# Kernel optimization log

Measured on AMD Instinct MI355X. Metric: run time of the kernel, lower is better.

The kernel has to match this reference:

```python
import jax, jax.numpy as jnp
import numpy as np
from jax import lax

# Grid / module constants (from init_kwargs)
D = 128        # spatial extent per axis (shape=[128,128,128])
CIN = 16       # in_channels
COUT = 32      # out_channels
K = 2          # kernel_size
S = 2          # stride
B = 2          # batch_size
N = 200000     # number of active voxels


def setup_inputs() -> dict:
    key = jax.random.key(0)
    k1, k2, k3, k4 = jax.random.split(key, 4)
    features = jax.random.normal(k1, (N, CIN), dtype=jnp.float32)
    coors = jax.random.randint(k2, (N, 4), 0, D)                  # [b, z, y, x]
    coors = coors.at[:, 0].set(coors[:, 0] % B)                    # batch ids in [0, B)
    # Learned params: SCN Convolution / Deconvolution weights (bias=False).
    W1 = jax.random.normal(k3, (COUT, CIN, K, K, K), dtype=jnp.float32) * 0.1
    W2 = jax.random.normal(k4, (CIN, COUT, K, K, K), dtype=jnp.float32) * 0.1
    return {"features": features, "W1": W1, "W2": W2, "coors": coors, "batch_size": B}


def reference(features, W1, W2, coors, batch_size):
    # scn.InputLayer: scatter point features onto the sparse voxel grid
    # (duplicate coords are summed). Inactive sites are exactly zero, so a
    # dense strided conv computes the same values as the rulebook
    # gather-GEMM-scatter at every active output site.
    b, z, y, x = coors[:, 0], coors[:, 1], coors[:, 2], coors[:, 3]
    dense = jnp.zeros((batch_size, CIN, D, D, D), dtype=features.dtype)
    dense = dense.at[b, :, z, y, x].add(features)                  # [B, CIN, D, D, D]

    dn = ("NCDHW", "OIDHW", "NCDHW")
    # scn.Convolution(ndim, CIN, COUT, K, S): valid strided conv -> [B, COUT, D//S, ...]
    h = lax.conv_general_dilated(dense, W1, window_strides=(S, S, S),
                                 padding="VALID", dimension_numbers=dn)
    # scn.Deconvolution(ndim, COUT, CIN, K, S): transposed conv back to [B, CIN, D, D, D]
    dec = lax.conv_general_dilated(h, W2, window_strides=(1, 1, 1),
                                   padding=[(K - 1, K - 1)] * 3,
                                   lhs_dilation=(S, S, S), dimension_numbers=dn)
    # Coupled deconv in SCN restores exactly the input active set; SparseToDense
    # then writes zeros everywhere else -> mask to the original active sites.
    mask = jnp.zeros((batch_size, 1, D, D, D), dtype=features.dtype)
    mask = mask.at[b, :, z, y, x].set(1.0)
    return dec * mask
```

## Files before the change

### kernel.cpp

```cpp
#include <hip/hip_runtime.h>


#define NPT_CH_SCATTER 32
#define NPT_CH_GATHER  16

__global__ __launch_bounds__(256) void scn_scatter_conv1(
    const float* __restrict__ feat, const float* __restrict__ W1,
    const int* __restrict__ coors, float* __restrict__ h, int npts)
{
    __shared__ float Ws[8 * 16 * 32];
    for (int i = threadIdx.x; i < 4096; i += 256) {
        int ic = i >> 7, rem = i & 127, cin = rem >> 3, p = rem & 7;
        Ws[(p << 9) | (cin << 5) | ic] = W1[i];
    }
    __syncthreads();

    int total = npts * NPT_CH_SCATTER;
    for (int idx = blockIdx.x * 256 + threadIdx.x; idx < total;
         idx += gridDim.x * 256) {
        int pid = idx >> 5, ic = idx & 31;
        int b = coors[pid * 4 + 0];
        int z = coors[pid * 4 + 1];
        int y = coors[pid * 4 + 2];
        int x = coors[pid * 4 + 3];
        int p = ((z & 1) << 2) | ((y & 1) << 1) | (x & 1);

        const float4* f4 = reinterpret_cast<const float4*>(feat + pid * 16);
        float4 a0 = f4[0], a1 = f4[1], a2 = f4[2], a3 = f4[3];

        const float* w = Ws + (p << 9) + ic;
        float s = 0.f;
        s += a0.x * w[0 << 5];  s += a0.y * w[1 << 5];
        s += a0.z * w[2 << 5];  s += a0.w * w[3 << 5];
        s += a1.x * w[4 << 5];  s += a1.y * w[5 << 5];
        s += a1.z * w[6 << 5];  s += a1.w * w[7 << 5];
        s += a2.x * w[8 << 5];  s += a2.y * w[9 << 5];
        s += a2.z * w[10 << 5]; s += a2.w * w[11 << 5];
        s += a3.x * w[12 << 5]; s += a3.y * w[13 << 5];
        s += a3.z * w[14 << 5]; s += a3.w * w[15 << 5];

        int cell = (b << 18) | ((z >> 1) << 12) | ((y >> 1) << 6) | (x >> 1);
        atomicAdd(&h[((size_t)cell << 5) | ic], s);
    }
}

__global__ __launch_bounds__(256) void scn_gather_deconv2(
    const float* __restrict__ h, const float* __restrict__ W2,
    const int* __restrict__ coors, float* __restrict__ out, int npts)
{
    __shared__ float Ws[8 * 32 * 16];
    for (int i = threadIdx.x; i < 4096; i += 256) {
        int oc = i >> 8, rem = i & 255, ic = rem >> 3, p = rem & 7;
        Ws[(p << 9) | (ic << 4) | oc] = W2[i];
    }
    __syncthreads();

    int total = npts * NPT_CH_GATHER;
    for (int idx = blockIdx.x * 256 + threadIdx.x; idx < total;
         idx += gridDim.x * 256) {
        int pid = idx >> 4, oc = idx & 15;
        int b = coors[pid * 4 + 0];
        int z = coors[pid * 4 + 1];
        int y = coors[pid * 4 + 2];
        int x = coors[pid * 4 + 3];
        int p = (((z & 1) ^ 1) << 2) | (((y & 1) ^ 1) << 1) | ((x & 1) ^ 1);

        int cell = (b << 18) | ((z >> 1) << 12) | ((y >> 1) << 6) | (x >> 1);
        const float4* h4 = reinterpret_cast<const float4*>(h + ((size_t)cell << 5));
        float4 h0 = h4[0], h1 = h4[1], h2 = h4[2], h3 = h4[3];
        float4 h5 = h4[4], h6 = h4[5], h7 = h4[6], h8 = h4[7];

        const float* w = Ws + (p << 9) + oc;
        float s = 0.f;
        s += h0.x * w[0 << 4];   s += h0.y * w[1 << 4];
        s += h0.z * w[2 << 4];   s += h0.w * w[3 << 4];
        s += h1.x * w[4 << 4];   s += h1.y * w[5 << 4];
        s += h1.z * w[6 << 4];   s += h1.w * w[7 << 4];
        s += h2.x * w[8 << 4];   s += h2.y * w[9 << 4];
        s += h2.z * w[10 << 4];  s += h2.w * w[11 << 4];
        s += h3.x * w[12 << 4];  s += h3.y * w[13 << 4];
        s += h3.z * w[14 << 4];  s += h3.w * w[15 << 4];
        s += h5.x * w[16 << 4];  s += h5.y * w[17 << 4];
        s += h5.z * w[18 << 4];  s += h5.w * w[19 << 4];
        s += h6.x * w[20 << 4];  s += h6.y * w[21 << 4];
        s += h6.z * w[22 << 4];  s += h6.w * w[23 << 4];
        s += h7.x * w[24 << 4];  s += h7.y * w[25 << 4];
        s += h7.z * w[26 << 4];  s += h7.w * w[27 << 4];
        s += h8.x * w[28 << 4];  s += h8.y * w[29 << 4];
        s += h8.z * w[30 << 4];  s += h8.w * w[31 << 4];

        size_t oidx = (size_t)(b * 16 + oc) * 2097152 + (size_t)z * 16384
                    + (size_t)y * 128 + (size_t)x;
        out[oidx] = s;
    }
}

extern "C" void kernel_launch(void* const* d_in, const int* in_sizes, int n_in,
                              void* d_out, int out_size, void* d_ws, size_t ws_size,
                              hipStream_t stream) {
    const float* feat  = (const float*)d_in[0];
    const float* W1    = (const float*)d_in[1];
    const float* W2    = (const float*)d_in[2];
    const int*   coors = (const int*)d_in[3];
    float*       out   = (float*)d_out;
    float*       h     = (float*)d_ws;
    int npts = in_sizes[0] / 16;

    const size_t h_bytes = (size_t)2 * 262144 * 32 * sizeof(float);

    hipMemsetAsync(d_out, 0, (size_t)out_size * sizeof(float), stream);
    hipMemsetAsync(d_ws, 0, h_bytes, stream);

    int t1 = npts * NPT_CH_SCATTER;
    int blocks1 = (t1 + 255) / 256;
    if (blocks1 > 4096) blocks1 = 4096;
    scn_scatter_conv1<<<blocks1, 256, 0, stream>>>(feat, W1, coors, h, npts);

    int t2 = npts * NPT_CH_GATHER;
    int blocks2 = (t2 + 255) / 256;
    if (blocks2 > 4096) blocks2 = 4096;
    scn_gather_deconv2<<<blocks2, 256, 0, stream>>>(h, W2, coors, out, npts);
}
```

Baseline: 430.9 us.

## Fuse output zero-fill with deconv gather using an occupancy bitmask

```diff
diff --git a/kernel.cpp b/kernel.cpp
--- a/kernel.cpp
+++ b/kernel.cpp
@@ -1,12 +1,15 @@
 #include <hip/hip_runtime.h>
+#include <stdint.h>
 
+#define H_BYTES ((size_t)2 * 262144 * 32 * sizeof(float))
+#define MASK_WORDS (2 * 65536)
 
-#define NPT_CH_SCATTER 32
-#define NPT_CH_GATHER  16
+typedef float f32x4 __attribute__((ext_vector_type(4)));
 
 __global__ __launch_bounds__(256) void scn_scatter_conv1(
     const float* __restrict__ feat, const float* __restrict__ W1,
-    const int* __restrict__ coors, float* __restrict__ h, int npts)
+    const int* __restrict__ coors, float* __restrict__ h,
+    uint32_t* __restrict__ maskw, int npts)
 {
     __shared__ float Ws[8 * 16 * 32];
     for (int i = threadIdx.x; i < 4096; i += 256) {
@@ -15,7 +18,7 @@
     }
     __syncthreads();
 
-    int total = npts * NPT_CH_SCATTER;
+    int total = npts * 32;
     for (int idx = blockIdx.x * 256 + threadIdx.x; idx < total;
          idx += gridDim.x * 256) {
         int pid = idx >> 5, ic = idx & 31;
@@ -25,28 +28,33 @@
         int x = coors[pid * 4 + 3];
         int p = ((z & 1) << 2) | ((y & 1) << 1) | (x & 1);
 
-        const float4* f4 = reinterpret_cast<const float4*>(feat + pid * 16);
-        float4 a0 = f4[0], a1 = f4[1], a2 = f4[2], a3 = f4[3];
+        const f32x4* f4 = reinterpret_cast<const f32x4*>(feat + pid * 16);
+        f32x4 a0 = f4[0], a1 = f4[1], a2 = f4[2], a3 = f4[3];
 
         const float* w = Ws + (p << 9) + ic;
         float s = 0.f;
-        s += a0.x * w[0 << 5];  s += a0.y * w[1 << 5];
-        s += a0.z * w[2 << 5];  s += a0.w * w[3 << 5];
-        s += a1.x * w[4 << 5];  s += a1.y * w[5 << 5];
-        s += a1.z * w[6 << 5];  s += a1.w * w[7 << 5];
-        s += a2.x * w[8 << 5];  s += a2.y * w[9 << 5];
-        s += a2.z * w[10 << 5]; s += a2.w * w[11 << 5];
-        s += a3.x * w[12 << 5]; s += a3.y * w[13 << 5];
-        s += a3.z * w[14 << 5]; s += a3.w * w[15 << 5];
+        s += a0[0] * w[0 << 5];   s += a0[1] * w[1 << 5];
+        s += a0[2] * w[2 << 5];   s += a0[3] * w[3 << 5];
+        s += a1[0] * w[4 << 5];   s += a1[1] * w[5 << 5];
+        s += a1[2] * w[6 << 5];   s += a1[3] * w[7 << 5];
+        s += a2[0] * w[8 << 5];   s += a2[1] * w[9 << 5];
+        s += a2[2] * w[10 << 5];  s += a2[3] * w[11 << 5];
+        s += a3[0] * w[12 << 5];  s += a3[1] * w[13 << 5];
+        s += a3[2] * w[14 << 5];  s += a3[3] * w[15 << 5];
 
         int cell = (b << 18) | ((z >> 1) << 12) | ((y >> 1) << 6) | (x >> 1);
         atomicAdd(&h[((size_t)cell << 5) | ic], s);
+
+        if (ic == 0) {
+            int voxel = (z << 14) | (y << 7) | x;
+            atomicOr(&maskw[(b << 16) | (voxel >> 5)], 1u << (voxel & 31));
+        }
     }
 }
 
-__global__ __launch_bounds__(256) void scn_gather_deconv2(
+__global__ __launch_bounds__(256) void scn_fill_deconv(
     const float* __restrict__ h, const float* __restrict__ W2,
-    const int* __restrict__ coors, float* __restrict__ out, int npts)
+    const uint32_t* __restrict__ maskw, float* __restrict__ out)
 {
     __shared__ float Ws[8 * 32 * 16];
     for (int i = threadIdx.x; i < 4096; i += 256) {
@@ -55,43 +63,47 @@
     }
     __syncthreads();
 
-    int total = npts * NPT_CH_GATHER;
-    for (int idx = blockIdx.x * 256 + threadIdx.x; idx < total;
-         idx += gridDim.x * 256) {
-        int pid = idx >> 4, oc = idx & 15;
-        int b = coors[pid * 4 + 0];
-        int z = coors[pid * 4 + 1];
-        int y = coors[pid * 4 + 2];
-        int x = coors[pid * 4 + 3];
-        int p = (((z & 1) ^ 1) << 2) | (((y & 1) ^ 1) << 1) | ((x & 1) ^ 1);
+    const int total4 = 16777216;
+    f32x4* out4 = reinterpret_cast<f32x4*>(out);
+    for (int o = blockIdx.x * 256 + threadIdx.x; o < total4;
+         o += gridDim.x * 256) {
+        int voxel4 = o & 524287;
+        int chan   = o >> 19;
+        int b = chan >> 4;
+        uint32_t mword = maskw[(b << 16) | (voxel4 >> 3)];
+        uint32_t nib = (mword >> ((voxel4 & 7) << 2)) & 0xFu;
 
-        int cell = (b << 18) | ((z >> 1) << 12) | ((y >> 1) << 6) | (x >> 1);
-        const float4* h4 = reinterpret_cast<const float4*>(h + ((size_t)cell << 5));
-        float4 h0 = h4[0], h1 = h4[1], h2 = h4[2], h3 = h4[3];
-        float4 h5 = h4[4], h6 = h4[5], h7 = h4[6], h8 = h4[7];
-
-        const float* w = Ws + (p << 9) + oc;
-        float s = 0.f;
-        s += h0.x * w[0 << 4];   s += h0.y * w[1 << 4];
-        s += h0.z * w[2 << 4];   s += h0.w * w[3 << 4];
-        s += h1.x * w[4 << 4];   s += h1.y * w[5 << 4];
-        s += h1.z * w[6 << 4];   s += h1.w * w[7 << 4];
-        s += h2.x * w[8 << 4];   s += h2.y * w[9 << 4];
-        s += h2.z * w[10 << 4];  s += h2.w * w[11 << 4];
-        s += h3.x * w[12 << 4];  s += h3.y * w[13 << 4];
-        s += h3.z * w[14 << 4];  s += h3.w * w[15 << 4];
-        s += h5.x * w[16 << 4];  s += h5.y * w[17 << 4];
-        s += h5.z * w[18 << 4];  s += h5.w * w[19 << 4];
-        s += h6.x * w[20 << 4];  s += h6.y * w[21 << 4];
-        s += h6.z * w[22 << 4];  s += h6.w * w[23 << 4];
-        s += h7.x * w[24 << 4];  s += h7.y * w[25 << 4];
-        s += h7.z * w[26 << 4];  s += h7.w * w[27 << 4];
-        s += h8.x * w[28 << 4];  s += h8.y * w[29 << 4];
-        s += h8.z * w[30 << 4];  s += h8.w * w[31 << 4];
-
-        size_t oidx = (size_t)(b * 16 + oc) * 2097152 + (size_t)z * 16384
-                    + (size_t)y * 128 + (size_t)x;
-        out[oidx] = s;
+        f32x4 r = {0.f, 0.f, 0.f, 0.f};
+        if (nib) {
+            int oc = chan & 15;
+            int x4 = voxel4 & 31;
+            int y  = (voxel4 >> 5) & 127;
+            int z  = voxel4 >> 12;
+            int cellzy = (b << 18) | ((z >> 1) << 12) | ((y >> 1) << 6);
+            int pzy = (((z & 1) ^ 1) << 2) | (((y & 1) ^ 1) << 1);
+            #pragma unroll
+            for (int j = 0; j < 4; ++j) {
+                if ((nib >> j) & 1u) {
+                    int x = (x4 << 2) | j;
+                    int p = pzy | ((x & 1) ^ 1);
+                    int cell = cellzy | (x >> 1);
+                    const f32x4* hc =
+                        reinterpret_cast<const f32x4*>(h + ((size_t)cell << 5));
+                    const float* w = Ws + (p << 9) + oc;
+                    float s = 0.f;
+                    #pragma unroll
+                    for (int q = 0; q < 8; ++q) {
+                        f32x4 hv = hc[q];
+                        s += hv[0] * w[(4 * q + 0) << 4];
+                        s += hv[1] * w[(4 * q + 1) << 4];
+                        s += hv[2] * w[(4 * q + 2) << 4];
+                        s += hv[3] * w[(4 * q + 3) << 4];
+                    }
+                    r[j] = s;
+                }
+            }
+        }
+        __builtin_nontemporal_store(r, out4 + o);
     }
 }
 
@@ -104,20 +116,15 @@
     const int*   coors = (const int*)d_in[3];
     float*       out   = (float*)d_out;
     float*       h     = (float*)d_ws;
+    uint32_t*    maskw = (uint32_t*)((char*)d_ws + H_BYTES);
     int npts = in_sizes[0] / 16;
 
-    const size_t h_bytes = (size_t)2 * 262144 * 32 * sizeof(float);
+    hipMemsetAsync(d_ws, 0, H_BYTES + MASK_WORDS * sizeof(uint32_t), stream);
 
-    hipMemsetAsync(d_out, 0, (size_t)out_size * sizeof(float), stream);
-    hipMemsetAsync(d_ws, 0, h_bytes, stream);
-
-    int t1 = npts * NPT_CH_SCATTER;
+    int t1 = npts * 32;
     int blocks1 = (t1 + 255) / 256;
     if (blocks1 > 4096) blocks1 = 4096;
-    scn_scatter_conv1<<<blocks1, 256, 0, stream>>>(feat, W1, coors, h, npts);
+    scn_scatter_conv1<<<blocks1, 256, 0, stream>>>(feat, W1, coors, h, maskw, npts);
 
-    int t2 = npts * NPT_CH_GATHER;
-    int blocks2 = (t2 + 255) / 256;
-    if (blocks2 > 4096) blocks2 = 4096;
-    scn_gather_deconv2<<<blocks2, 256, 0, stream>>>(h, W2, coors, out, npts);
+    scn_fill_deconv<<<8192, 256, 0, stream>>>(h, W2, maskw, out);
 }
```

New measurement: 545.5 us. +26.6%, slower.
